# Performance work log

Hardware: AMD Instinct MI355X
Metric: run time of the kernel (lower is better)

The kernel has to match this reference:

```python
import jax, jax.numpy as jnp
import numpy as np

N = 50000      # nodes
E = 800000     # edges (avg degree 16)
DIN = 256      # input_dim
DH = 128       # hidden_dim
ALPHA_LOGIT = 0.6190392084062235  # logit(0.65)


def setup_inputs() -> dict:
    key = jax.random.key(0)
    ks = jax.random.split(key, 12)
    f = lambda k, s: jax.random.normal(k, s, dtype=jnp.float32)
    return {
        "x": f(ks[0], (N, DIN)),
        "edge_index": jax.random.randint(ks[1], (2, E), 0, N, dtype=jnp.int32),
        "reranker_scores": f(ks[2], (N,)),
        # input_proj
        "Wp": f(ks[3], (DIN, DH)) * 0.02, "bp": jnp.zeros((DH,), jnp.float32),
        # SAGEConv 0: lin_l (aggregated neighbors, with bias), lin_r (root, no bias)
        "Wl0": f(ks[4], (DIN, DH)) * 0.02, "bl0": jnp.zeros((DH,), jnp.float32),
        "Wr0": f(ks[5], (DIN, DH)) * 0.02,
        # SAGEConv 1
        "Wl1": f(ks[6], (DH, DH)) * 0.02, "bl1": jnp.zeros((DH,), jnp.float32),
        "Wr1": f(ks[7], (DH, DH)) * 0.02,
        # score head MLP
        "W1": f(ks[8], (DH, DH // 2)) * 0.02, "b1": jnp.zeros((DH // 2,), jnp.float32),
        "W2": f(ks[9], (DH // 2, 1)) * 0.02, "b2": jnp.zeros((1,), jnp.float32),
        "alpha_logit": jnp.float32(ALPHA_LOGIT),
    }


def _sage_conv(h, src, dst, Wl, bl, Wr):
    # PyG SAGEConv (aggr='mean', root_weight=True):
    # out = lin_l(mean_{j in N(i)} h_j) + lin_r(h_i)
    msg = h[src]                                             # [E, d] gather
    agg = jax.ops.segment_sum(msg, dst, num_segments=N)      # [N, d]
    cnt = jax.ops.segment_sum(jnp.ones((src.shape[0],), h.dtype), dst, num_segments=N)
    agg = agg / jnp.maximum(cnt, 1.0)[:, None]               # mean; isolated nodes -> 0
    return agg @ Wl + bl + h @ Wr


def reference(x, edge_index, reranker_scores, Wp, bp, Wl0, bl0, Wr0,
              Wl1, bl1, Wr1, W1, b1, W2, b2, alpha_logit):
    src, dst = edge_index[0], edge_index[1]
    # norm_type='none' -> no input normalization; eval mode -> dropout is identity
    residual = x @ Wp + bp                                   # [N, DH]
    h = jax.nn.relu(_sage_conv(x, src, dst, Wl0, bl0, Wr0)) + residual
    h = jax.nn.relu(_sage_conv(h, src, dst, Wl1, bl1, Wr1)) + h
    gnn_scores = (jax.nn.relu(h @ W1 + b1) @ W2 + b2)[:, 0]  # [N]
    alpha = jax.nn.sigmoid(alpha_logit)
    return alpha * reranker_scores + (1.0 - alpha) * gnn_scores
```

## Files before the change

### kernel.cpp

```cpp
#include <hip/hip_runtime.h>
#include <hip/hip_bf16.h>


#define DIN 256
#define DH 128
#define NPB 256
#define LOG_NPB 8
#define NBMAX 256
#define EPB 2048
#define JL (EPB/256)
#define SLOTS 8192

typedef __attribute__((ext_vector_type(8))) short short8;
typedef __attribute__((ext_vector_type(4))) float float4v;
typedef __attribute__((ext_vector_type(2))) float float2v;

__device__ inline ushort f2b(float f){
  unsigned u = __float_as_uint(f);
  u = (u + 0x7fffu + ((u >> 16) & 1u)) >> 16;
  return (ushort)u;
}
__device__ inline float blo(unsigned v){ return __uint_as_float(v << 16); }
__device__ inline float bhi(unsigned v){ return __uint_as_float(v & 0xffff0000u); }
__device__ inline float b2f(ushort v){ return __uint_as_float(((unsigned)v) << 16); }
__device__ inline short8 pack8(float4 f0, float4 f1){
  short8 v;
  v[0]=(short)f2b(f0.x); v[1]=(short)f2b(f0.y); v[2]=(short)f2b(f0.z); v[3]=(short)f2b(f0.w);
  v[4]=(short)f2b(f1.x); v[5]=(short)f2b(f1.y); v[6]=(short)f2b(f1.z); v[7]=(short)f2b(f1.w);
  return v;
}
__device__ inline void glds16(const ushort* g, ushort* l){
  __builtin_amdgcn_global_load_lds((const __attribute__((address_space(1))) void*)g,
                                   (__attribute__((address_space(3))) void*)l, 16, 0, 0);
}
__device__ inline unsigned char enc8(float v){
  return (unsigned char)(__builtin_amdgcn_cvt_pk_fp8_f32(v, v, 0, false) & 0xFF);
}
__device__ inline float2v dec8(unsigned u){
  return __builtin_amdgcn_cvt_pk_f32_fp8((int)u, false);
}

__device__ inline void gather16x2b(const unsigned char* __restrict__ a8,
    const ushort* __restrict__ adj, int pA, int eA, int pB, int eB, int lane,
    float& aA, float& aB)
{
  while (pA < eA || pB < eB){
    unsigned char uA[16], uB[16];
    bool dA = pA < eA, dB = pB < eB;
    if (dA){
      #pragma unroll
      for (int j=0;j<16;j++){
        int ix = __builtin_amdgcn_readfirstlane((int)adj[pA+j]);
        uA[j] = a8[(size_t)ix*64 + lane];
      }
    }
    if (dB){
      #pragma unroll
      for (int j=0;j<16;j++){
        int ix = __builtin_amdgcn_readfirstlane((int)adj[pB+j]);
        uB[j] = a8[(size_t)ix*64 + lane];
      }
    }
    if (dA){
      #pragma unroll
      for (int j=0;j<8;j++){
        unsigned u = (unsigned)uA[2*j] | ((unsigned)uA[2*j+1] << 8);
        float2v f = dec8(u);
        aA += f[0] + f[1];
      }
      pA += 16;
    }
    if (dB){
      #pragma unroll
      for (int j=0;j<8;j++){
        unsigned u = (unsigned)uB[2*j] | ((unsigned)uB[2*j+1] << 8);
        float2v f = dec8(u);
        aB += f[0] + f[1];
      }
      pB += 16;
    }
  }
}

__global__ __launch_bounds__(256) void fused_front(
    const float* __restrict__ x, int N, ushort* __restrict__ xb, int nstripe,
    const float* __restrict__ Wp, const float* __restrict__ Wl0, const float* __restrict__ Wr0,
    const float* __restrict__ Wl1, const float* __restrict__ Wr1, const float* __restrict__ W1,
    ushort* __restrict__ Wpf, ushort* __restrict__ Wl0f, ushort* __restrict__ Wr0f,
    ushort* __restrict__ Wl1f, ushort* __restrict__ Wr1f, ushort* __restrict__ W1f,
    const int* __restrict__ src, const int* __restrict__ dst, int E, int NB,
    int* __restrict__ bucketCnt, int* __restrict__ pairS, int* __restrict__ pairD,
    int nPart, int nConv)
{
  __shared__ int hist[NBMAX], lbase[NBMAX], gbase[NBMAX], lcur[NBMAX], sc[NBMAX];
  __shared__ int ls[EPB], ld[EPB];
  int bid = blockIdx.x;
  int t = threadIdx.x;

  if (bid < nPart){
    int base = bid * EPB;
    int cntE = E - base; if (cntE > EPB) cntE = EPB;
    for (int i=t;i<NB;i+=256) hist[i]=0;
    __syncthreads();
    int myS[JL], myD[JL];
    #pragma unroll
    for (int j=0;j<JL;j++){
      int e = base + j*256 + t;
      if (e < E){ myS[j]=src[e]; myD[j]=dst[e]; atomicAdd(&hist[myD[j]>>LOG_NPB],1); }
      else myD[j] = -1;
    }
    __syncthreads();
    if (t < NBMAX) sc[t] = (t < NB)? hist[t] : 0;
    __syncthreads();
    for (int st=1; st<NBMAX; st<<=1){
      int v = 0;
      if (t < NBMAX && t >= st) v = sc[t-st];
      __syncthreads();
      if (t < NBMAX) sc[t] += v;
      __syncthreads();
    }
    if (t < NB){
      int excl = (t>0)? sc[t-1] : 0;
      lbase[t] = excl; lcur[t] = excl;
      gbase[t] = atomicAdd(&bucketCnt[t], hist[t]);
    }
    __syncthreads();
    #pragma unroll
    for (int j=0;j<JL;j++){
      if (myD[j] >= 0){
        int b = myD[j] >> LOG_NPB;
        int p = atomicAdd(&lcur[b], 1);
        ls[p] = myS[j]; ld[p] = myD[j];
      }
    }
    __syncthreads();
    for (int i=t;i<cntE;i+=256){
      int d = ld[i];
      int b = d >> LOG_NPB;
      int p = gbase[b] + (i - lbase[b]);
      if (p < SLOTS){
        pairS[(size_t)b*SLOTS + p] = ls[i];
        pairD[(size_t)b*SLOTS + p] = d;
      }
    }
  } else if (bid < nPart + nConv){
    int gi = (bid - nPart)*256 + t;
    if (gi < nstripe*512){
      int L = gi & 63, ks = (gi>>6)&7, s = gi>>9;
      int row = s*16 + (L&15);
      int k = ks*32 + (L>>4)*8;
      short8 v;
      if (row < N){
        const float* p = x + (size_t)row*DIN + k;
        v = pack8(*(const float4*)p, *(const float4*)(p+4));
      } else {
        #pragma unroll
        for (int j=0;j<8;j++) v[j]=0;
      }
      *(short8*)(xb + (size_t)gi*8) = v;
    }
  } else {
    int gi = (bid - nPart - nConv)*256 + t;
    if (gi < 17408){
      const float* sw; ushort* dw; int cols, b0;
      if      (gi <  4096){ sw=Wp;  dw=Wpf;  cols=128; b0=0; }
      else if (gi <  8192){ sw=Wl0; dw=Wl0f; cols=128; b0=4096; }
      else if (gi < 12288){ sw=Wr0; dw=Wr0f; cols=128; b0=8192; }
      else if (gi < 14336){ sw=Wl1; dw=Wl1f; cols=128; b0=12288; }
      else if (gi < 16384){ sw=Wr1; dw=Wr1f; cols=128; b0=14336; }
      else                { sw=W1;  dw=W1f;  cols=64;  b0=16384; }
      int i = gi - b0;
      int ln = i & 63, g = i >> 6;
      int ntq = cols >> 4;
      int nt = g % ntq, ks = g / ntq;
      int col = nt*16 + (ln & 15);
      int k0 = ks*32 + (ln >> 4)*8;
      short8 v;
      #pragma unroll
      for (int j=0;j<8;j++) v[j] = (short)f2b(sw[(size_t)(k0+j)*cols + col]);
      *(short8*)(dw + (size_t)i*8) = v;
    }
  }
}

__global__ __launch_bounds__(256) void gemm0_csr(
    const ushort* __restrict__ xb, int N, int nstripe, int ngemm, int nbuck,
    const ushort* __restrict__ Wpf, const ushort* __restrict__ Wl0f, const ushort* __restrict__ Wr0f,
    const float* __restrict__ bp,
    ushort* __restrict__ xp, unsigned char* __restrict__ q8lo, unsigned char* __restrict__ q8hi,
    ushort* __restrict__ xr0,
    const int* __restrict__ bucketCnt, const int* __restrict__ pairS, const int* __restrict__ pairD,
    int* __restrict__ off, int* __restrict__ deg, ushort* __restrict__ adj)
{
  __shared__ __align__(16) ushort smem[32768];
  int bid = blockIdx.x, t = threadIdx.x;

  if (bid >= nbuck){
    int g = bid - nbuck;
    int xcd = g & 7, jj = g >> 3;
    int mat = jj % 3;
    int b = xcd + 8*(jj/3);
    int nblk = ngemm / 3;
    const ushort* Wf = (mat==0)? Wpf : (mat==1)? Wl0f : Wr0f;
    int w = t>>6, lane = t&63, lq = lane&15, quad = lane>>4;
    #pragma unroll
    for (int j=0;j<16;j++){
      int gg = w + j*4;
      glds16(Wf + (size_t)gg*512 + lane*8, smem + gg*512);
    }
    __syncthreads();
    float bias[8];
    #pragma unroll
    for (int nt=0;nt<8;nt++) bias[nt] = (mat==0)? bp[nt*16 + lq] : 0.f;
    int nchunk = (nstripe + 3) >> 2;

#define LOADAV(AV, cc) do { \
    int stripe_ = (cc)*4 + w; \
    if (stripe_ < nstripe){ \
      _Pragma("unroll") \
      for (int ks=0;ks<8;ks++) \
        AV[ks] = *(const short8*)(xb + ((size_t)stripe_*8 + ks)*512 + lane*8); \
    } \
  } while(0)

#define COMPSTORE(AV, cc) do { \
    int stripe_ = (cc)*4 + w; \
    if (stripe_ < nstripe){ \
      int row0_ = stripe_*16; \
      float4v acc_[8]; \
      _Pragma("unroll") for (int nt=0;nt<8;nt++){ \
        _Pragma("unroll") for (int r=0;r<4;r++) acc_[nt][r]=0.f; } \
      _Pragma("unroll") for (int ks=0;ks<8;ks++){ \
        _Pragma("unroll") for (int nt=0;nt<8;nt++){ \
          short8 bf_ = *(const short8*)(smem + (size_t)((ks*8+nt)*64 + lane)*8); \
          acc_[nt] = __builtin_amdgcn_mfma_f32_16x16x32_bf16(AV[ks], bf_, acc_[nt], 0,0,0); \
        } \
      } \
      if (mat == 1){ \
        _Pragma("unroll") for (int nt=0;nt<8;nt++) \
        _Pragma("unroll") for (int r=0;r<4;r++){ \
          int row_ = row0_ + quad*4 + r; \
          if (row_ < N){ \
            if (nt < 4) q8lo[(size_t)row_*64 + nt*16 + lq] = enc8(acc_[nt][r]); \
            else        q8hi[(size_t)row_*64 + (nt-4)*16 + lq] = enc8(acc_[nt][r]); \
          } \
        } \
      } else { \
        ushort* Y_ = (mat==0)? xp : xr0; \
        _Pragma("unroll") for (int nt=0;nt<8;nt++) \
        _Pragma("unroll") for (int r=0;r<4;r++){ \
          int row_ = row0_ + quad*4 + r; \
          if (row_ < N) Y_[(size_t)row_*128 + nt*16 + lq] = f2b(acc_[nt][r] + bias[nt]); \
        } \
      } \
    } \
  } while(0)

    short8 avA[8], avB[8];
    int c = b;
    if (c < nchunk){
      LOADAV(avA, c);
      while (true){
        int cn = c + nblk;
        if (cn < nchunk) LOADAV(avB, cn);
        COMPSTORE(avA, c);
        c = cn;
        if (c >= nchunk) break;
        cn = c + nblk;
        if (cn < nchunk) LOADAV(avA, cn);
        COMPSTORE(avB, c);
        c = cn;
        if (c >= nchunk) break;
      }
    }
#undef LOADAV
#undef COMPSTORE
  } else {
    int b = bid;
    int* cnt  = (int*)smem;
    int* offl = cnt + 256;
    int* s1   = offl + 257;
    ushort* win = (ushort*)(s1 + 256);
    int node0 = b * NPB;
    int base  = b * SLOTS;
    int ce = bucketCnt[b]; if (ce > SLOTS) ce = SLOTS;
    int ce4 = ce & ~3;
    cnt[t] = 0;
    __syncthreads();
    for (int i = t*4; i < ce4; i += 1024){
      int4 dd = *(const int4*)(pairD + base + i);
      atomicAdd(&cnt[dd.x - node0], 1);
      atomicAdd(&cnt[dd.y - node0], 1);
      atomicAdd(&cnt[dd.z - node0], 1);
      atomicAdd(&cnt[dd.w - node0], 1);
    }
    for (int i = ce4 + t; i < ce; i += 256)
      atomicAdd(&cnt[pairD[(size_t)base+i] - node0], 1);
    __syncthreads();
    int a = cnt[t];
    int pa = (a + 15) & ~15;
    s1[t] = pa;
    __syncthreads();
    for (int st=1; st<256; st<<=1){
      int v = (t>=st)? s1[t-st] : 0;
      __syncthreads();
      s1[t] += v;
      __syncthreads();
    }
    int excl = (t>0)? s1[t-1] : 0;
    offl[t] = excl;
    int ptotal = s1[255]; if (ptotal > SLOTS) ptotal = SLOTS;
    int node = node0 + t;
    if (node < N){ off[node] = base + excl; deg[node] = a; }
    __syncthreads();
    for (int i=t;i<ptotal;i+=256) win[i] = (ushort)N;
    __syncthreads();
    for (int i = t*4; i < ce4; i += 1024){
      int4 dd = *(const int4*)(pairD + base + i);
      int4 ss = *(const int4*)(pairS + base + i);
      int p0 = atomicAdd(&offl[dd.x - node0], 1); if (p0 < SLOTS) win[p0] = (ushort)ss.x;
      int p1 = atomicAdd(&offl[dd.y - node0], 1); if (p1 < SLOTS) win[p1] = (ushort)ss.y;
      int p2 = atomicAdd(&offl[dd.z - node0], 1); if (p2 < SLOTS) win[p2] = (ushort)ss.z;
      int p3 = atomicAdd(&offl[dd.w - node0], 1); if (p3 < SLOTS) win[p3] = (ushort)ss.w;
    }
    for (int i = ce4 + t; i < ce; i += 256){
      int dd = pairD[(size_t)base+i];
      int p = atomicAdd(&offl[dd - node0], 1);
      if (p < SLOTS) win[p] = (ushort)pairS[(size_t)base+i];
    }
    __syncthreads();
    for (int i=t;i<ptotal;i+=256) adj[(size_t)base+i] = win[i];
  }
}

__global__ __launch_bounds__(256) void combine_f8h(
    const unsigned char* __restrict__ q8lo, const unsigned char* __restrict__ q8hi,
    const ushort* __restrict__ rootsrc, const ushort* __restrict__ ressrc,
    const float* __restrict__ bias,
    const int* __restrict__ off, const int* __restrict__ deg,
    const ushort* __restrict__ adj, ushort* __restrict__ out, int n, int nbh)
{
  int t = threadIdx.x;
  int d = t & 63, w = t >> 6;
  int b = blockIdx.x;
  int half = (b >= nbh) ? 1 : 0;
  int nA = (b - half*nbh)*8 + w*2, nB = nA + 1;
  if (nA >= n) return;
  const unsigned char* a8 = half ? q8hi : q8lo;
  int hd = half*64 + d;
  bool vB = nB < n;
  ushort rtA = rootsrc[(size_t)nA*128 + hd];
  ushort rsA = ressrc[(size_t)nA*128 + hd];
  ushort rtB = 0, rsB = 0;
  int pA = off[nA], cA = deg[nA], eA = pA + ((cA + 15) & ~15);
  int pB = 0, cB = 0, eB = 0;
  if (vB){
    rtB = rootsrc[(size_t)nB*128 + hd];
    rsB = ressrc[(size_t)nB*128 + hd];
    pB = off[nB]; cB = deg[nB]; eB = pB + ((cB + 15) & ~15);
  }
  float aA = 0.f, aB = 0.f;
  gather16x2b(a8, adj, pA, eA, pB, eB, d, aA, aB);
  float bv = bias[hd];
  float invA = 1.f / (float)((cA > 1)? cA : 1);
  float o0 = fmaxf(aA*invA + bv + b2f(rtA), 0.f) + b2f(rsA);
  out[(size_t)nA*128 + hd] = f2b(o0);
  if (vB){
    float invB = 1.f / (float)((cB > 1)? cB : 1);
    float o1 = fmaxf(aB*invB + bv + b2f(rtB), 0.f) + b2f(rsB);
    out[(size_t)nB*128 + hd] = f2b(o1);
  }
}

__global__ __launch_bounds__(256) void gemm1_wres(
    const ushort* __restrict__ h, int N,
    const ushort* __restrict__ Wl1f, const ushort* __restrict__ Wr1f,
    unsigned char* __restrict__ q8lo, unsigned char* __restrict__ q8hi,
    ushort* __restrict__ hr1)
{
  __shared__ __align__(16) ushort Bs[32768];
  int t = threadIdx.x, w = t>>6, lane = t&63, lq = lane&15, quad = lane>>4;
  int tile = blockIdx.x;
  #pragma unroll
  for (int j=0;j<16;j++){
    int r = w + j*4;
    int m = r>>5, g = r&31;
    const ushort* Wm = m ? Wr1f : Wl1f;
    glds16(Wm + (size_t)g*512 + lane*8, Bs + r*512);
  }
  short8 av[2][4];
  int row0 = tile*128 + w*32;
  #pragma unroll
  for (int mt=0;mt<2;mt++){
    int row = row0 + mt*16 + lq; if (row >= N) row = N-1;
    #pragma unroll
    for (int ks=0;ks<4;ks++)
      av[mt][ks] = *(const short8*)(h + (size_t)row*128 + ks*32 + quad*8);
  }
  __syncthreads();
  #pragma unroll
  for (int m=0;m<2;m++){
    float4v acc[2][8];
    #pragma unroll
    for (int i=0;i<2;i++)
      #pragma unroll
      for (int j=0;j<8;j++)
        #pragma unroll
        for (int r=0;r<4;r++) acc[i][j][r] = 0.f;
    #pragma unroll
    for (int ks=0;ks<4;ks++){
      #pragma unroll
      for (int nt=0;nt<8;nt++){
        short8 bf = *(const short8*)(Bs + ((m*32 + ks*8 + nt)*64 + lane)*8);
        acc[0][nt] = __builtin_amdgcn_mfma_f32_16x16x32_bf16(av[0][ks], bf, acc[0][nt], 0,0,0);
        acc[1][nt] = __builtin_amdgcn_mfma_f32_16x16x32_bf16(av[1][ks], bf, acc[1][nt], 0,0,0);
      }
    }
    #pragma unroll
    for (int mt=0;mt<2;mt++){
      #pragma unroll
      for (int r=0;r<4;r++){
        int row = row0 + mt*16 + quad*4 + r;
        if (row < N){
          if (m == 0){
            #pragma unroll
            for (int nt=0;nt<8;nt++){
              if (nt < 4) q8lo[(size_t)row*64 + nt*16 + lq] = enc8(acc[mt][nt][r]);
              else        q8hi[(size_t)row*64 + (nt-4)*16 + lq] = enc8(acc[mt][nt][r]);
            }
          } else {
            #pragma unroll
            for (int nt=0;nt<8;nt++)
              hr1[(size_t)row*128 + nt*16 + lq] = f2b(acc[mt][nt][r]);
          }
        }
      }
    }
  }
}

__global__ __launch_bounds__(256) void head_mlp(
    const ushort* __restrict__ h2, int n,
    const ushort* __restrict__ W1f, const float* __restrict__ b1,
    const float* __restrict__ W2, const float* __restrict__ b2,
    const float* __restrict__ alogit, const float* __restrict__ rer,
    float* __restrict__ out)
{
  __shared__ __align__(16) ushort W1s[8192];
  int t = threadIdx.x, w = t>>6, lane = t&63, lq = lane&15, quad = lane>>4;
  #pragma unroll
  for (int j=0;j<4;j++){
    int g = w + j*4;
    glds16(W1f + (size_t)g*512 + lane*8, W1s + g*512);
  }
  int row0 = blockIdx.x*128 + w*32;
  short8 av[2][4];
  #pragma unroll
  for (int mt=0;mt<2;mt++){
    int row = row0 + mt*16 + lq; if (row >= n) row = n-1;
    #pragma unroll
    for (int ks=0;ks<4;ks++)
      av[mt][ks] = *(const short8*)(h2 + (size_t)row*128 + ks*32 + quad*8);
  }
  __syncthreads();
  float4v acc[2][4];
  #pragma unroll
  for (int mt=0;mt<2;mt++)
    #pragma unroll
    for (int nt=0;nt<4;nt++)
      #pragma unroll
      for (int r=0;r<4;r++) acc[mt][nt][r] = 0.f;
  #pragma unroll
  for (int ks=0;ks<4;ks++){
    #pragma unroll
    for (int nt=0;nt<4;nt++){
      short8 bf = *(const short8*)(W1s + ((ks*4 + nt)*64 + lane)*8);
      acc[0][nt] = __builtin_amdgcn_mfma_f32_16x16x32_bf16(av[0][ks], bf, acc[0][nt], 0,0,0);
      acc[1][nt] = __builtin_amdgcn_mfma_f32_16x16x32_bf16(av[1][ks], bf, acc[1][nt], 0,0,0);
    }
  }
  float al = alogit[0];
  float a  = 1.f / (1.f + __expf(-al));
  #pragma unroll
  for (int mt=0;mt<2;mt++){
    float pw[4] = {0.f,0.f,0.f,0.f};
    #pragma unroll
    for (int nt=0; nt<4; nt++){
      int c = nt*16 + lq;
      float w2 = W2[c];
      float bb = b1[c];
      #pragma unroll
      for (int r=0; r<4; r++)
        pw[r] += fmaxf(acc[mt][nt][r] + bb, 0.f) * w2;
    }
    #pragma unroll
    for (int mask=1; mask<16; mask<<=1){
      #pragma unroll
      for (int r=0; r<4; r++)
        pw[r] += __shfl_xor(pw[r], mask);
    }
    if (lq == 0){
      #pragma unroll
      for (int r=0; r<4; r++){
        int row = row0 + mt*16 + quad*4 + r;
        if (row < n)
          out[row] = a * rer[row] + (1.f - a) * (pw[r] + b2[0]);
      }
    }
  }
}

extern "C" void kernel_launch(void* const* d_in, const int* in_sizes, int n_in,
                              void* d_out, int out_size, void* d_ws, size_t ws_size,
                              hipStream_t stream)
{
  (void)n_in; (void)out_size; (void)ws_size;
  const float* x    = (const float*)d_in[0];
  const int*   ei   = (const int*)d_in[1];
  const float* rer  = (const float*)d_in[2];
  const float* Wp   = (const float*)d_in[3];
  const float* bp   = (const float*)d_in[4];
  const float* Wl0  = (const float*)d_in[5];
  const float* bl0  = (const float*)d_in[6];
  const float* Wr0  = (const float*)d_in[7];
  const float* Wl1  = (const float*)d_in[8];
  const float* bl1  = (const float*)d_in[9];
  const float* Wr1  = (const float*)d_in[10];
  const float* W1   = (const float*)d_in[11];
  const float* b1   = (const float*)d_in[12];
  const float* W2   = (const float*)d_in[13];
  const float* b2   = (const float*)d_in[14];
  const float* alogit = (const float*)d_in[15];

  const int N = in_sizes[2];
  const int E = in_sizes[1] / 2;
  const int* src = ei;
  const int* dst = ei + E;
  const int NB = (N + NPB - 1) / NPB;
  const int nstripe = (N + 15) / 16;
  const int ntile = (N + 127) / 128;
  const int nPart = (E + EPB - 1) / EPB;
  const int nConv = (nstripe*512 + 255)/256;
  const int nbh = (N + 7) / 8;

  ushort* U = (ushort*)d_ws;
  ushort* xb  = U;
  ushort* xp  = xb + (size_t)nstripe*512*8;
  ushort* xr0 = xp  + (size_t)N*DH;
  ushort* h   = xr0 + (size_t)N*DH;
  unsigned char* q8lo = (unsigned char*)(h + (size_t)N*DH);
  unsigned char* q8hi = q8lo + (size_t)(N+1)*64;
  ushort* Wpf  = (ushort*)(q8hi + (size_t)(N+1)*64);
  ushort* Wl0f = Wpf  + (size_t)4096*8;
  ushort* Wr0f = Wl0f + (size_t)4096*8;
  ushort* Wl1f = Wr0f + (size_t)4096*8;
  ushort* Wr1f = Wl1f + (size_t)2048*8;
  ushort* W1f  = Wr1f + (size_t)2048*8;
  int* I = (int*)(W1f + (size_t)1024*8);
  int* bucketCnt = I;
  int* off   = bucketCnt + NBMAX;
  int* deg   = off + N;
  int* pairS = deg + N;
  int* pairD = pairS + (size_t)NB*SLOTS;
  ushort* adj = (ushort*)(pairD + (size_t)NB*SLOTS);
  ushort* h2  = xb;

  hipMemsetAsync(bucketCnt, 0, NBMAX*sizeof(int), stream);
  hipMemsetAsync(q8lo + (size_t)N*64, 0, 64, stream);
  hipMemsetAsync(q8hi + (size_t)N*64, 0, 64, stream);

  fused_front<<<nPart + nConv + 68, 256, 0, stream>>>(
      x, N, xb, nstripe, Wp, Wl0, Wr0, Wl1, Wr1, W1,
      Wpf, Wl0f, Wr0f, Wl1f, Wr1f, W1f,
      src, dst, E, NB, bucketCnt, pairS, pairD, nPart, nConv);

  gemm0_csr<<<NB + 768, 256, 0, stream>>>(
      xb, N, nstripe, 768, NB, Wpf, Wl0f, Wr0f, bp, xp, q8lo, q8hi, xr0,
      bucketCnt, pairS, pairD, off, deg, adj);

  combine_f8h<<<2*nbh, 256, 0, stream>>>(q8lo, q8hi, xr0, xp, bl0, off, deg, adj, h, N, nbh);

  gemm1_wres<<<ntile, 256, 0, stream>>>(h, N, Wl1f, Wr1f, q8lo, q8hi, xr0);

  combine_f8h<<<2*nbh, 256, 0, stream>>>(q8lo, q8hi, xr0, h, bl1, off, deg, adj, h2, N, nbh);

  head_mlp<<<ntile, 256, 0, stream>>>(h2, N, W1f, b1, W2, b2, alogit, rer, (float*)d_out);
}
```

Measured before the change: 252.2 us.

## Split edge gather across wave halves with 2-byte loads in combine kernel

Reworks the fp8 neighbor-gather in combine_f8h. Each wave half now handles alternate edges: it reads 16 adjacency indices with two vector loads and takes the even or odd 16-bit index by shifting. It then loads 2 fp8 features per lane instead of 1, and the two halves are reduced with a cross-half shuffle. The epilogue is remapped so each half writes one node with packed 2-element loads and stores. The goal is fewer, wider memory instructions and no per-edge readfirstlane scalar index loads, at the cost of extra shuffle and select logic.

```diff
diff --git a/kernel.cpp b/kernel.cpp
--- a/kernel.cpp
+++ b/kernel.cpp
@@ -38,48 +38,6 @@
 }
 __device__ inline float2v dec8(unsigned u){
   return __builtin_amdgcn_cvt_pk_f32_fp8((int)u, false);
-}
-
-__device__ inline void gather16x2b(const unsigned char* __restrict__ a8,
-    const ushort* __restrict__ adj, int pA, int eA, int pB, int eB, int lane,
-    float& aA, float& aB)
-{
-  while (pA < eA || pB < eB){
-    unsigned char uA[16], uB[16];
-    bool dA = pA < eA, dB = pB < eB;
-    if (dA){
-      #pragma unroll
-      for (int j=0;j<16;j++){
-        int ix = __builtin_amdgcn_readfirstlane((int)adj[pA+j]);
-        uA[j] = a8[(size_t)ix*64 + lane];
-      }
-    }
-    if (dB){
-      #pragma unroll
-      for (int j=0;j<16;j++){
-        int ix = __builtin_amdgcn_readfirstlane((int)adj[pB+j]);
-        uB[j] = a8[(size_t)ix*64 + lane];
-      }
-    }
-    if (dA){
-      #pragma unroll
-      for (int j=0;j<8;j++){
-        unsigned u = (unsigned)uA[2*j] | ((unsigned)uA[2*j+1] << 8);
-        float2v f = dec8(u);
-        aA += f[0] + f[1];
-      }
-      pA += 16;
-    }
-    if (dB){
-      #pragma unroll
-      for (int j=0;j<8;j++){
-        unsigned u = (unsigned)uB[2*j] | ((unsigned)uB[2*j+1] << 8);
-        float2v f = dec8(u);
-        aB += f[0] + f[1];
-      }
-      pB += 16;
-    }
-  }
 }
 
 __global__ __launch_bounds__(256) void fused_front(
@@ -340,35 +298,74 @@
     const int* __restrict__ off, const int* __restrict__ deg,
     const ushort* __restrict__ adj, ushort* __restrict__ out, int n, int nbh)
 {
-  int t = threadIdx.x;
-  int d = t & 63, w = t >> 6;
+  int t = threadIdx.x, w = t>>6, lane = t&63;
+  int sub = lane & 31, hi = lane >> 5;
   int b = blockIdx.x;
   int half = (b >= nbh) ? 1 : 0;
   int nA = (b - half*nbh)*8 + w*2, nB = nA + 1;
   if (nA >= n) return;
   const unsigned char* a8 = half ? q8hi : q8lo;
-  int hd = half*64 + d;
   bool vB = nB < n;
-  ushort rtA = rootsrc[(size_t)nA*128 + hd];
-  ushort rsA = ressrc[(size_t)nA*128 + hd];
-  ushort rtB = 0, rsB = 0;
   int pA = off[nA], cA = deg[nA], eA = pA + ((cA + 15) & ~15);
   int pB = 0, cB = 0, eB = 0;
+  if (vB){ pB = off[nB]; cB = deg[nB]; eB = pB + ((cB + 15) & ~15); }
+  int boff = sub*2;
+  int sh = hi << 4;
+  float2v aA = {0.f,0.f}, aB = {0.f,0.f};
+  while (pA < eA || pB < eB){
+    bool dA = pA < eA, dB = pB < eB;
+    ushort uA[8], uB[8];
+    if (dA){
+      uint4 x0 = *(const uint4*)(adj + pA);
+      uint4 x1 = *(const uint4*)(adj + pA + 8);
+      unsigned wv[8] = {x0.x,x0.y,x0.z,x0.w,x1.x,x1.y,x1.z,x1.w};
+      #pragma unroll
+      for (int j=0;j<8;j++){
+        unsigned ix = (wv[j] >> sh) & 0xffffu;
+        uA[j] = *(const ushort*)(a8 + (size_t)ix*64 + boff);
+      }
+    }
+    if (dB){
+      uint4 x0 = *(const uint4*)(adj + pB);
+      uint4 x1 = *(const uint4*)(adj + pB + 8);
+      unsigned wv[8] = {x0.x,x0.y,x0.z,x0.w,x1.x,x1.y,x1.z,x1.w};
+      #pragma unroll
+      for (int j=0;j<8;j++){
+        unsigned ix = (wv[j] >> sh) & 0xffffu;
+        uB[j] = *(const ushort*)(a8 + (size_t)ix*64 + boff);
+      }
+    }
+    if (dA){
+      #pragma unroll
+      for (int j=0;j<8;j++) aA += dec8(uA[j]);
+      pA += 16;
+    }
+    if (dB){
+      #pragma unroll
+      for (int j=0;j<8;j++) aB += dec8(uB[j]);
+      pB += 16;
+    }
+  }
+  aA[0] += __shfl_xor(aA[0], 32);
+  aA[1] += __shfl_xor(aA[1], 32);
   if (vB){
-    rtB = rootsrc[(size_t)nB*128 + hd];
-    rsB = ressrc[(size_t)nB*128 + hd];
-    pB = off[nB]; cB = deg[nB]; eB = pB + ((cB + 15) & ~15);
-  }
-  float aA = 0.f, aB = 0.f;
-  gather16x2b(a8, adj, pA, eA, pB, eB, d, aA, aB);
-  float bv = bias[hd];
-  float invA = 1.f / (float)((cA > 1)? cA : 1);
-  float o0 = fmaxf(aA*invA + bv + b2f(rtA), 0.f) + b2f(rsA);
-  out[(size_t)nA*128 + hd] = f2b(o0);
-  if (vB){
-    float invB = 1.f / (float)((cB > 1)? cB : 1);
-    float o1 = fmaxf(aB*invB + bv + b2f(rtB), 0.f) + b2f(rsB);
-    out[(size_t)nB*128 + hd] = f2b(o1);
+    aB[0] += __shfl_xor(aB[0], 32);
+    aB[1] += __shfl_xor(aB[1], 32);
+  }
+  int nodeT = hi ? nB : nA;
+  int cT    = hi ? cB : cA;
+  float s0  = hi ? aB[0] : aA[0];
+  float s1v = hi ? aB[1] : aA[1];
+  bool vT   = hi ? vB : true;
+  if (vT){
+    int hd = half*64 + boff;
+    unsigned rt = *(const unsigned*)(rootsrc + (size_t)nodeT*128 + hd);
+    unsigned rs = *(const unsigned*)(ressrc  + (size_t)nodeT*128 + hd);
+    float2 bv = *(const float2*)(bias + hd);
+    float inv = 1.f / (float)((cT > 1)? cT : 1);
+    float o0 = fmaxf(s0 *inv + bv.x + blo(rt), 0.f) + blo(rs);
+    float o1 = fmaxf(s1v*inv + bv.y + bhi(rt), 0.f) + bhi(rs);
+    *(unsigned*)(out + (size_t)nodeT*128 + hd) = (unsigned)f2b(o0) | ((unsigned)f2b(o1) << 16);
   }
 }
 
```

New measurement: 237.8 us. -5.7%, faster.
